# Kernel tuning notes

Hardware: AMD Instinct MI355X
Metric: run time of the kernel (lower is better)

## Reference

```python
import jax, jax.numpy as jnp
import numpy as np
import math

B, T, E, K, V = 64, 512, 512, 512, 512


def setup_inputs() -> dict:
    key = jax.random.key(0)
    ks = jax.random.split(key, 7)
    s = 1.0 / math.sqrt(E)
    return {
        "x": jax.random.normal(ks[0], (B, T, E), dtype=jnp.float32),
        "Wq": jax.random.normal(ks[1], (E, K), dtype=jnp.float32) * s,
        "bq": jnp.zeros((K,), dtype=jnp.float32),
        "Wk": jax.random.normal(ks[2], (E, K), dtype=jnp.float32) * s,
        "bk": jnp.zeros((K,), dtype=jnp.float32),
        "Wv": jax.random.normal(ks[3], (E, V), dtype=jnp.float32) * s,
        "bv": jnp.zeros((V,), dtype=jnp.float32),
    }


def reference(x, Wq, bq, Wk, bk, Wv, bv):
    # Linear projections (N, T, E) -> (N, T, K/V)
    q = x @ Wq + bq
    k = x @ Wk + bk
    v = x @ Wv + bv
    # weight_pos_graph(query, keys) interpreted as Q K^T: (N, T, T)
    scores = jnp.einsum("btd,bsd->bts", q, k)
    # mask[j, i] = 1 if i > j  -> strict upper triangle masked to -inf (causal)
    mask = jnp.triu(jnp.ones((T, T), dtype=bool), k=1)
    scores = jnp.where(mask, -jnp.inf, scores)
    # NOTE: original softmaxes over dim=1 (the query/row axis), not dim=-1
    attn = jax.nn.softmax(scores / math.sqrt(K), axis=1)
    # bmm(attn, values): (N, T, T) @ (N, T, V) -> (N, T, V)
    return jnp.einsum("bts,bsv->btv", attn, v)
```

## Files before the change

kernel.cpp:

```cpp
#include <hip/hip_runtime.h>
#include <hip/hip_bf16.h>
#include <math.h>

#define B_DIM 64
#define T_DIM 512
#define E_DIM 512

typedef __bf16 bf16_t;
typedef bf16_t bf16x8 __attribute__((ext_vector_type(8)));
typedef float  f32x4  __attribute__((ext_vector_type(4)));

typedef unsigned char __attribute__((address_space(1))) uc_g;
typedef unsigned char __attribute__((address_space(3))) uc_l;

__device__ __forceinline__ void gl_lds16(const void* g, void* l) {
  __builtin_amdgcn_global_load_lds((const uc_g*)g, (uc_l*)l, 16, 0, 0);
}

__global__ __launch_bounds__(256)
void prep_kernel(const float* __restrict__ x,
                 const float* __restrict__ Wq, const float* __restrict__ Wk,
                 const float* __restrict__ Wv,
                 const float* __restrict__ bq, const float* __restrict__ bk,
                 const float* __restrict__ bv,
                 bf16_t* __restrict__ xb, bf16_t* __restrict__ WTall,
                 float* __restrict__ bcat, float* __restrict__ Dsum) {
  __shared__ float tile[32][33];
  const int bx = blockIdx.x;
  const int t = threadIdx.x;
  if (bx < 8192) {
    const size_t i = (size_t)bx * 256 + t;
    const float4 a = ((const float4*)x)[i * 2];
    const float4 b = ((const float4*)x)[i * 2 + 1];
    bf16x8 o;
    o[0] = (bf16_t)a.x; o[1] = (bf16_t)a.y; o[2] = (bf16_t)a.z; o[3] = (bf16_t)a.w;
    o[4] = (bf16_t)b.x; o[5] = (bf16_t)b.y; o[6] = (bf16_t)b.z; o[7] = (bf16_t)b.w;
    *(bf16x8*)(xb + i * 8) = o;
  } else if (bx < 8960) {
    const int bid = bx - 8192;
    const int z = bid >> 8;
    const int tl = bid & 255;
    const int c0 = (tl & 15) * 32, r0 = (tl >> 4) * 32;
    const float* W = z == 0 ? Wq : (z == 1 ? Wk : Wv);
    bf16_t* O = WTall + (size_t)z * 512 * E_DIM;
    const int tx = t & 31, ty = t >> 5;
#pragma unroll
    for (int i = 0; i < 4; ++i)
      tile[ty + i * 8][tx] = W[(size_t)(r0 + ty + i * 8) * E_DIM + c0 + tx];
    __syncthreads();
#pragma unroll
    for (int i = 0; i < 4; ++i)
      O[(size_t)(c0 + ty + i * 8) * E_DIM + r0 + tx] = (bf16_t)tile[tx][ty + i * 8];
  } else if (bx == 8960) {
#pragma unroll
    for (int i = t; i < 1536; i += 256)
      bcat[i] = i < 512 ? bq[i] : (i < 1024 ? bk[i - 512] : bv[i - 1024]);
  } else {
    const int i = (bx - 8961) * 256 + t;
    ((float4*)Dsum)[i] = make_float4(0.f, 0.f, 0.f, 0.f);
  }
}

__global__ __launch_bounds__(512) void vtr_kernel(const bf16_t* __restrict__ Vb,
                                                  const float* __restrict__ Dsum,
                                                  bf16_t* __restrict__ VT, int ldv) {
  const int b = blockIdx.z;
  __shared__ bf16_t tile[64][65];
  const int tx = threadIdx.x, ty = threadIdx.y;
  const bf16_t* src = Vb + (size_t)b * T_DIM * ldv;
  const float* Ds = Dsum + (size_t)b * T_DIM;
  bf16_t* dst = VT + (size_t)b * T_DIM * T_DIM;
  const int r0 = blockIdx.y * 64, c0 = blockIdx.x * 64;
#pragma unroll
  for (int i = 0; i < 8; ++i) {
    const int s = r0 + ty + i * 8;
    const float inv = 1.0f / Ds[s];
    tile[ty + i * 8][tx] = (bf16_t)((float)src[(size_t)s * ldv + c0 + tx] * inv);
  }
  __syncthreads();
#pragma unroll
  for (int i = 0; i < 8; ++i)
    dst[(size_t)(c0 + ty + i * 8) * T_DIM + r0 + tx] = tile[tx][ty + i * 8];
}

__global__ __launch_bounds__(512)
void gemm8p_qkv(const bf16_t* __restrict__ A, const bf16_t* __restrict__ Bt,
                bf16_t* __restrict__ C, const float* __restrict__ bias) {
  __shared__ bf16_t lds[65536];
  const int tid = threadIdx.x;

  const int lin = blockIdx.x;
  const int nl = (lin & 7) * 96 + (lin >> 3);
  const int bm = nl / 6, bn = nl - bm * 6;

  const int sg = (tid & 3) ^ ((tid >> 3) & 3);
  const bf16_t* gA = A + ((long)bm * 256 + (tid >> 2)) * 512 + sg * 8;
  const bf16_t* gB = Bt + ((long)bn * 256 + (tid >> 2)) * 512 + sg * 8;

#define STG(T, regoff, gp, kh) {                                          \
    bf16_t* d_ = &lds[(((T) & 1) << 15) + (regoff) + tid * 8];            \
    gl_lds16((gp) + (long)(T) * 64 + (kh) * 32, d_);                      \
    gl_lds16((gp) + (long)(T) * 64 + (kh) * 32 + (long)128 * 512, d_ + 4096); }
#define STG_Ak0(T) STG(T, 0,     gA, 0)
#define STG_Ak1(T) STG(T, 8192,  gA, 1)
#define STG_Bk0(T) STG(T, 16384, gB, 0)
#define STG_Bk1(T) STG(T, 24576, gB, 1)

  const int l15 = tid & 15, lk = (tid >> 4) & 3;
  const int w = tid >> 6, wr = w >> 2, wc = w & 3;
  int aoffs[8], boffs[4];
#pragma unroll
  for (int mm = 0; mm < 8; ++mm) {
    const int row = wr * 128 + mm * 16 + l15;
    aoffs[mm] = row * 32 + (lk ^ ((row >> 1) & 3)) * 8;
  }
#pragma unroll
  for (int n = 0; n < 4; ++n) {
    const int row = wc * 64 + n * 16 + l15;
    boffs[n] = row * 32 + (lk ^ ((row >> 1) & 3)) * 8;
  }

  f32x4 acc[8][4] = {};

  STG_Bk0(0); STG_Ak0(0); STG_Bk1(0); STG_Ak1(0);
  STG_Bk0(1); STG_Ak0(1); STG_Bk1(1);
  asm volatile("s_waitcnt vmcnt(6)" ::: "memory");
  asm volatile("s_barrier" ::: "memory");

#define MFMA16(BASE, AF, BF)                                                    \
  __builtin_amdgcn_s_setprio(1);                                                \
  _Pragma("unroll") for (int m_ = 0; m_ < 4; ++m_)                              \
    _Pragma("unroll") for (int n_ = 0; n_ < 4; ++n_)                            \
      acc[(BASE) + m_][n_] =                                                    \
        __builtin_amdgcn_mfma_f32_16x16x32_bf16(AF[m_], BF[n_], acc[(BASE) + m_][n_], 0, 0, 0); \
  __builtin_amdgcn_s_setprio(0);

  for (int kt = 0; kt < 8; ++kt) {
    const int bb = (kt & 1) << 15;
    bf16x8 a[4], b0[4], b1[4];

#pragma unroll
    for (int n = 0; n < 4; ++n) b0[n] = *(const bf16x8*)&lds[bb + 16384 + boffs[n]];
#pragma unroll
    for (int m = 0; m < 4; ++m) a[m] = *(const bf16x8*)&lds[bb + aoffs[m]];
    if (kt + 1 < 8) STG_Ak1(kt + 1);
    asm volatile("s_barrier" ::: "memory");
    MFMA16(0, a, b0);
    asm volatile("s_barrier" ::: "memory");

#pragma unroll
    for (int m = 0; m < 4; ++m) a[m] = *(const bf16x8*)&lds[bb + aoffs[4 + m]];
    if (kt + 2 < 8) STG_Bk0(kt + 2);
    asm volatile("s_barrier" ::: "memory");
    MFMA16(4, a, b0);
    asm volatile("s_barrier" ::: "memory");

#pragma unroll
    for (int n = 0; n < 4; ++n) b1[n] = *(const bf16x8*)&lds[bb + 24576 + boffs[n]];
#pragma unroll
    for (int m = 0; m < 4; ++m) a[m] = *(const bf16x8*)&lds[bb + 8192 + aoffs[m]];
    if (kt + 2 < 8) STG_Ak0(kt + 2);
    asm volatile("s_barrier" ::: "memory");
    MFMA16(0, a, b1);
    asm volatile("s_barrier" ::: "memory");

#pragma unroll
    for (int m = 0; m < 4; ++m) a[m] = *(const bf16x8*)&lds[bb + 8192 + aoffs[4 + m]];
    if (kt + 2 < 8) {
      STG_Bk1(kt + 2);
      asm volatile("s_waitcnt vmcnt(6)" ::: "memory");
    } else if (kt + 1 < 8) {
      asm volatile("s_waitcnt vmcnt(0)" ::: "memory");
    }
    asm volatile("s_barrier" ::: "memory");
    MFMA16(4, a, b1);
    asm volatile("s_barrier" ::: "memory");
  }
#undef MFMA16
#undef STG_Ak0
#undef STG_Ak1
#undef STG_Bk0
#undef STG_Bk1
#undef STG

#pragma unroll
  for (int mm = 0; mm < 8; ++mm) {
    const long row0 = (long)bm * 256 + wr * 128 + mm * 16 + lk * 4;
#pragma unroll
    for (int n = 0; n < 4; ++n) {
      const int col = bn * 256 + wc * 64 + n * 16 + l15;
      const float bv = bias[col];
#pragma unroll
      for (int r = 0; r < 4; ++r)
        C[(row0 + r) * 1536 + col] = (bf16_t)(acc[mm][n][r] + bv);
    }
  }
}

template <int EPI>
__global__ __launch_bounds__(512)
void gemm_p(const bf16_t* __restrict__ A, const bf16_t* __restrict__ Bt,
            void* __restrict__ Cv, const float* __restrict__ bias,
            float* __restrict__ Dsum,
            int lda, int ldb, int ldc, long sA, long sB, long sC, float scale) {
  __shared__ bf16_t lds[3][12288];
  const int tid = threadIdx.x;

  int bm, bn, bz, NT;
  bm = blockIdx.x; bn = blockIdx.y; bz = blockIdx.z;
  if (EPI == 1 && 2 * bn > bm) return;
  NT = (EPI == 2) ? (bm + 1) * 4 : 16;

  const bf16_t* Ab = A + bz * sA + (long)bm * 128 * lda;
  const bf16_t* Bb = Bt + bz * sB + (long)bn * 256 * ldb;

  const int strow = tid >> 2, stg = tid & 3;
  const int sgg = stg ^ ((strow >> 1) & 3);
  const bf16_t* gA  = Ab + (long)strow * lda + sgg * 8;
  const bf16_t* gB0 = Bb + (long)strow * ldb + sgg * 8;
  const bf16_t* gB1 = gB0 + (long)128 * ldb;

#define STAGE(kt, buf) { gl_lds16(gA  + (long)(kt) * 32, &lds[buf][tid * 8]);        \
                         gl_lds16(gB0 + (long)(kt) * 32, &lds[buf][4096 + tid * 8]); \
                         gl_lds16(gB1 + (long)(kt) * 32, &lds[buf][8192 + tid * 8]); }

  const int l15 = tid & 15, lk = (tid >> 4) & 3;
  const int w = tid >> 6, wr = w >> 2, wc = w & 3;
  int aoff[4], boff[4];
#pragma unroll
  for (int m = 0; m < 4; ++m) {
    const int row = wr * 64 + m * 16 + l15;
    aoff[m] = row * 32 + (lk ^ ((row >> 1) & 3)) * 8;
  }
#pragma unroll
  for (int n = 0; n < 4; ++n) {
    const int row = wc * 64 + n * 16 + l15;
    boff[n] = 4096 + row * 32 + (lk ^ ((row >> 1) & 3)) * 8;
  }

  f32x4 acc[4][4] = {};

  STAGE(0, 0); STAGE(1, 1);
  asm volatile("s_waitcnt vmcnt(3)" ::: "memory");
  asm volatile("s_barrier" ::: "memory");

  int cb = 0;
  for (int kt = 0; kt < NT; ++kt) {
    bf16x8 af[4], bfr[4];
#pragma unroll
    for (int m = 0; m < 4; ++m) af[m] = *(const bf16x8*)&lds[cb][aoff[m]];
#pragma unroll
    for (int n = 0; n < 4; ++n) bfr[n] = *(const bf16x8*)&lds[cb][boff[n]];
    const int sb = (cb == 0) ? 2 : cb - 1;
    if (kt + 2 < NT) {
      STAGE(kt + 2, sb);
      asm volatile("s_waitcnt vmcnt(3)" ::: "memory");
    } else if (kt + 2 == NT) {
      asm volatile("s_waitcnt vmcnt(0)" ::: "memory");
    }
    asm volatile("s_barrier" ::: "memory");
    __builtin_amdgcn_s_setprio(1);
#pragma unroll
    for (int m = 0; m < 4; ++m)
#pragma unroll
      for (int n = 0; n < 4; ++n)
        acc[m][n] = __builtin_amdgcn_mfma_f32_16x16x32_bf16(af[m], bfr[n], acc[m][n], 0, 0, 0);
    __builtin_amdgcn_s_setprio(0);
    asm volatile("s_barrier" ::: "memory");
    cb = (cb == 2) ? 0 : cb + 1;
  }
#undef STAGE

  if constexpr (EPI == 1) {
    bf16_t* C = (bf16_t*)Cv + bz * sC;
    float ts[4] = {0.f, 0.f, 0.f, 0.f};
#pragma unroll
    for (int m = 0; m < 4; ++m) {
      const long row0 = (long)bm * 128 + wr * 64 + m * 16 + lk * 4;
#pragma unroll
      for (int n = 0; n < 4; ++n) {
        const int col = bn * 256 + wc * 64 + n * 16 + l15;
#pragma unroll
        for (int r = 0; r < 4; ++r) {
          const long row = row0 + r;
          float e = 0.f;
          if (col <= row) e = __expf(acc[m][n][r] * scale);
          const bf16_t eb = (bf16_t)e;
          C[row * (long)ldc + col] = eb;
          ts[n] += (float)eb;
        }
      }
    }
#pragma unroll
    for (int n = 0; n < 4; ++n) {
      ts[n] += __shfl_xor(ts[n], 16);
      ts[n] += __shfl_xor(ts[n], 32);
    }
    float* colsum = (float*)&lds[0][0];
    if (tid < 256) colsum[tid] = 0.f;
    __syncthreads();
    if (lk == 0) {
#pragma unroll
      for (int n = 0; n < 4; ++n)
        atomicAdd(&colsum[wc * 64 + n * 16 + l15], ts[n]);
    }
    __syncthreads();
    if (tid < 256)
      atomicAdd(&Dsum[(long)bz * T_DIM + bn * 256 + tid], colsum[tid]);
  } else {
    float* C = (float*)Cv + bz * sC;
#pragma unroll
    for (int m = 0; m < 4; ++m) {
      const long row0 = (long)bm * 128 + wr * 64 + m * 16 + lk * 4;
#pragma unroll
      for (int n = 0; n < 4; ++n) {
        const int col = bn * 256 + wc * 64 + n * 16 + l15;
#pragma unroll
        for (int r = 0; r < 4; ++r)
          C[(row0 + r) * (long)ldc + col] = acc[m][n][r];
      }
    }
  }
}

extern "C" void kernel_launch(void* const* d_in, const int* in_sizes, int n_in,
                              void* d_out, int out_size, void* d_ws, size_t ws_size,
                              hipStream_t stream) {
  const float* x  = (const float*)d_in[0];
  const float* Wq = (const float*)d_in[1];
  const float* bq = (const float*)d_in[2];
  const float* Wk = (const float*)d_in[3];
  const float* bk = (const float*)d_in[4];
  const float* Wv = (const float*)d_in[5];
  const float* bv = (const float*)d_in[6];
  float* out = (float*)d_out;

  char* ws = (char*)d_ws;
  const size_t SZ = (size_t)B_DIM * T_DIM * E_DIM * 2;
  bf16_t* xb    = (bf16_t*)(ws);
  bf16_t* P     = (bf16_t*)(ws);
  bf16_t* qkv   = (bf16_t*)(ws + SZ);
  bf16_t* vT    = (bf16_t*)(ws + SZ + 3 * SZ);
  bf16_t* WTall = (bf16_t*)(ws + 5 * SZ);
  float*  bcat  = (float*)(ws + 5 * SZ + 1572864);
  float*  Dsum  = (float*)(ws + 5 * SZ + 1572864 + 8192);

  const long sQKV = (long)T_DIM * 1536;
  const long bstr = (long)T_DIM * T_DIM;
  const float scale = 1.0f / sqrtf((float)E_DIM);

  prep_kernel<<<dim3(8993), dim3(256), 0, stream>>>(
      x, Wq, Wk, Wv, bq, bk, bv, xb, WTall, bcat, Dsum);
  gemm8p_qkv<<<dim3(768), dim3(512), 0, stream>>>(xb, WTall, qkv, bcat);
  gemm_p<1><<<dim3(4, 2, B_DIM), dim3(512), 0, stream>>>(
      qkv, qkv + 512, P, nullptr, Dsum, 1536, 1536, T_DIM, sQKV, sQKV, bstr, scale);
  vtr_kernel<<<dim3(8, 8, B_DIM), dim3(64, 8), 0, stream>>>(qkv + 1024, Dsum, vT, 1536);
  gemm_p<2><<<dim3(4, 2, B_DIM), dim3(512), 0, stream>>>(
      P, vT, out, nullptr, nullptr, 512, 512, T_DIM, bstr, bstr, bstr, 1.f);
}
```

Baseline: 273.5 us.

## Fuse column softmax normalization into scores kernel and write V transposed from projection

The scores kernel now computes all 512 query rows for a 128-key column block per workgroup. This lets it reduce column sums in LDS and normalize P directly, with no global Dsum atomics and no separate normalization pass. The projection GEMM switches to 128x256 tiles with a 3-buffer pipeline and writes the V slice transposed directly into vT, which removes the vtr_kernel launch and its extra read/write pass. The cost is that upper-triangle waves sit idle in the scores kernel, and there are only 256 scores workgroups, which lowers occupancy.

```diff
diff --git a/kernel.cpp b/kernel.cpp
--- a/kernel.cpp
+++ b/kernel.cpp
@@ -8,6 +8,7 @@
 
 typedef __bf16 bf16_t;
 typedef bf16_t bf16x8 __attribute__((ext_vector_type(8)));
+typedef bf16_t bf16x4 __attribute__((ext_vector_type(4)));
 typedef float  f32x4  __attribute__((ext_vector_type(4)));
 
 typedef unsigned char __attribute__((address_space(1))) uc_g;
@@ -24,7 +25,7 @@
                  const float* __restrict__ bq, const float* __restrict__ bk,
                  const float* __restrict__ bv,
                  bf16_t* __restrict__ xb, bf16_t* __restrict__ WTall,
-                 float* __restrict__ bcat, float* __restrict__ Dsum) {
+                 float* __restrict__ bcat) {
   __shared__ float tile[32][33];
   const int bx = blockIdx.x;
   const int t = threadIdx.x;
@@ -51,63 +52,141 @@
 #pragma unroll
     for (int i = 0; i < 4; ++i)
       O[(size_t)(c0 + ty + i * 8) * E_DIM + r0 + tx] = (bf16_t)tile[tx][ty + i * 8];
-  } else if (bx == 8960) {
+  } else {
 #pragma unroll
     for (int i = t; i < 1536; i += 256)
       bcat[i] = i < 512 ? bq[i] : (i < 1024 ? bk[i - 512] : bv[i - 1024]);
-  } else {
-    const int i = (bx - 8961) * 256 + t;
-    ((float4*)Dsum)[i] = make_float4(0.f, 0.f, 0.f, 0.f);
-  }
-}
-
-__global__ __launch_bounds__(512) void vtr_kernel(const bf16_t* __restrict__ Vb,
-                                                  const float* __restrict__ Dsum,
-                                                  bf16_t* __restrict__ VT, int ldv) {
-  const int b = blockIdx.z;
-  __shared__ bf16_t tile[64][65];
-  const int tx = threadIdx.x, ty = threadIdx.y;
-  const bf16_t* src = Vb + (size_t)b * T_DIM * ldv;
-  const float* Ds = Dsum + (size_t)b * T_DIM;
-  bf16_t* dst = VT + (size_t)b * T_DIM * T_DIM;
-  const int r0 = blockIdx.y * 64, c0 = blockIdx.x * 64;
-#pragma unroll
-  for (int i = 0; i < 8; ++i) {
-    const int s = r0 + ty + i * 8;
-    const float inv = 1.0f / Ds[s];
-    tile[ty + i * 8][tx] = (bf16_t)((float)src[(size_t)s * ldv + c0 + tx] * inv);
-  }
-  __syncthreads();
-#pragma unroll
-  for (int i = 0; i < 8; ++i)
-    dst[(size_t)(c0 + ty + i * 8) * T_DIM + r0 + tx] = tile[tx][ty + i * 8];
+  }
 }
 
 __global__ __launch_bounds__(512)
-void gemm8p_qkv(const bf16_t* __restrict__ A, const bf16_t* __restrict__ Bt,
-                bf16_t* __restrict__ C, const float* __restrict__ bias) {
-  __shared__ bf16_t lds[65536];
+void proj_kernel(const bf16_t* __restrict__ A, const bf16_t* __restrict__ Bt,
+                 bf16_t* __restrict__ qkv, bf16_t* __restrict__ vT,
+                 const float* __restrict__ bias) {
+  __shared__ bf16_t lds[3][12288];
   const int tid = threadIdx.x;
 
   const int lin = blockIdx.x;
-  const int nl = (lin & 7) * 96 + (lin >> 3);
+  const int nl = (lin & 7) * 192 + (lin >> 3);
   const int bm = nl / 6, bn = nl - bm * 6;
 
-  const int sg = (tid & 3) ^ ((tid >> 3) & 3);
-  const bf16_t* gA = A + ((long)bm * 256 + (tid >> 2)) * 512 + sg * 8;
-  const bf16_t* gB = Bt + ((long)bn * 256 + (tid >> 2)) * 512 + sg * 8;
-
-#define STG(T, regoff, gp, kh) {                                          \
-    bf16_t* d_ = &lds[(((T) & 1) << 15) + (regoff) + tid * 8];            \
-    gl_lds16((gp) + (long)(T) * 64 + (kh) * 32, d_);                      \
-    gl_lds16((gp) + (long)(T) * 64 + (kh) * 32 + (long)128 * 512, d_ + 4096); }
-#define STG_Ak0(T) STG(T, 0,     gA, 0)
-#define STG_Ak1(T) STG(T, 8192,  gA, 1)
-#define STG_Bk0(T) STG(T, 16384, gB, 0)
-#define STG_Bk1(T) STG(T, 24576, gB, 1)
+  const bf16_t* Ab = A + (long)bm * 128 * 512;
+  const bf16_t* Bb = Bt + (long)bn * 256 * 512;
+
+  const int strow = tid >> 2, stg = tid & 3;
+  const int sgg = stg ^ ((strow >> 1) & 3);
+  const bf16_t* gA  = Ab + (long)strow * 512 + sgg * 8;
+  const bf16_t* gB0 = Bb + (long)strow * 512 + sgg * 8;
+  const bf16_t* gB1 = gB0 + (long)128 * 512;
+
+#define STAGE(kt, buf) { gl_lds16(gA  + (long)(kt) * 32, &lds[buf][tid * 8]);        \
+                         gl_lds16(gB0 + (long)(kt) * 32, &lds[buf][4096 + tid * 8]); \
+                         gl_lds16(gB1 + (long)(kt) * 32, &lds[buf][8192 + tid * 8]); }
 
   const int l15 = tid & 15, lk = (tid >> 4) & 3;
   const int w = tid >> 6, wr = w >> 2, wc = w & 3;
+  int aoff[4], boff[4];
+#pragma unroll
+  for (int m = 0; m < 4; ++m) {
+    const int row = wr * 64 + m * 16 + l15;
+    aoff[m] = row * 32 + (lk ^ ((row >> 1) & 3)) * 8;
+  }
+#pragma unroll
+  for (int n = 0; n < 4; ++n) {
+    const int row = wc * 64 + n * 16 + l15;
+    boff[n] = 4096 + row * 32 + (lk ^ ((row >> 1) & 3)) * 8;
+  }
+
+  f32x4 acc[4][4] = {};
+
+  STAGE(0, 0); STAGE(1, 1);
+  asm volatile("s_waitcnt vmcnt(3)" ::: "memory");
+  asm volatile("s_barrier" ::: "memory");
+
+  int cb = 0;
+  for (int kt = 0; kt < 16; ++kt) {
+    bf16x8 af[4], bfr[4];
+#pragma unroll
+    for (int m = 0; m < 4; ++m) af[m] = *(const bf16x8*)&lds[cb][aoff[m]];
+#pragma unroll
+    for (int n = 0; n < 4; ++n) bfr[n] = *(const bf16x8*)&lds[cb][boff[n]];
+    const int sb = (cb == 0) ? 2 : cb - 1;
+    if (kt + 2 < 16) {
+      STAGE(kt + 2, sb);
+      asm volatile("s_waitcnt vmcnt(3)" ::: "memory");
+    } else if (kt + 2 == 16) {
+      asm volatile("s_waitcnt vmcnt(0)" ::: "memory");
+    }
+    asm volatile("s_barrier" ::: "memory");
+    __builtin_amdgcn_s_setprio(1);
+#pragma unroll
+    for (int m = 0; m < 4; ++m)
+#pragma unroll
+      for (int n = 0; n < 4; ++n)
+        acc[m][n] = __builtin_amdgcn_mfma_f32_16x16x32_bf16(af[m], bfr[n], acc[m][n], 0, 0, 0);
+    __builtin_amdgcn_s_setprio(0);
+    asm volatile("s_barrier" ::: "memory");
+    cb = (cb == 2) ? 0 : cb + 1;
+  }
+#undef STAGE
+
+  if (bn < 4) {
+#pragma unroll
+    for (int m = 0; m < 4; ++m) {
+      const long row0 = (long)bm * 128 + wr * 64 + m * 16 + lk * 4;
+#pragma unroll
+      for (int n = 0; n < 4; ++n) {
+        const int col = bn * 256 + wc * 64 + n * 16 + l15;
+        const float bv = bias[col];
+#pragma unroll
+        for (int r = 0; r < 4; ++r)
+          qkv[(row0 + r) * 1536L + col] = (bf16_t)(acc[m][n][r] + bv);
+      }
+    }
+  } else {
+#pragma unroll
+    for (int m = 0; m < 4; ++m) {
+      const long row0 = (long)bm * 128 + wr * 64 + m * 16 + lk * 4;
+      const long b = row0 >> 9;
+      const int s0 = (int)(row0 & 511);
+#pragma unroll
+      for (int n = 0; n < 4; ++n) {
+        const int col = bn * 256 + wc * 64 + n * 16 + l15;
+        const float bv = bias[col];
+        const int vc = col - 1024;
+        bf16x4 o;
+#pragma unroll
+        for (int r = 0; r < 4; ++r) o[r] = (bf16_t)(acc[m][n][r] + bv);
+        *(bf16x4*)(vT + b * 262144 + (long)vc * 512 + s0) = o;
+      }
+    }
+  }
+}
+
+__global__ __launch_bounds__(512)
+void scores_kernel(const bf16_t* __restrict__ qkv, bf16_t* __restrict__ P,
+                   float scale) {
+  __shared__ bf16_t lds[3][20480];
+  const int tid = threadIdx.x;
+  const int bn = blockIdx.x;
+  const int bz = blockIdx.y;
+  const bf16_t* q = qkv + (long)bz * T_DIM * 1536;
+  const bf16_t* k = q + 512;
+
+  const int strow = tid >> 2, stg = tid & 3;
+  const int sg = stg ^ ((strow >> 1) & 3);
+  const bf16_t* gA = q + (long)strow * 1536 + sg * 8;
+  const bf16_t* gB = k + ((long)bn * 128 + strow) * 1536 + sg * 8;
+
+#define STAGE(kt, buf) {                                                            \
+    _Pragma("unroll") for (int i_ = 0; i_ < 4; ++i_)                                \
+      gl_lds16(gA + (long)(kt) * 32 + (long)i_ * 128 * 1536,                        \
+               &lds[buf][i_ * 4096 + tid * 8]);                                     \
+    gl_lds16(gB + (long)(kt) * 32, &lds[buf][16384 + tid * 8]); }
+
+  const int l15 = tid & 15, lk = (tid >> 4) & 3;
+  const int w = tid >> 6, wr = w >> 1, wc = w & 1;
+  const int active = (wr >= bn);
   int aoffs[8], boffs[4];
 #pragma unroll
   for (int mm = 0; mm < 8; ++mm) {
@@ -117,108 +196,116 @@
 #pragma unroll
   for (int n = 0; n < 4; ++n) {
     const int row = wc * 64 + n * 16 + l15;
-    boffs[n] = row * 32 + (lk ^ ((row >> 1) & 3)) * 8;
+    boffs[n] = 16384 + row * 32 + (lk ^ ((row >> 1) & 3)) * 8;
   }
 
   f32x4 acc[8][4] = {};
 
-  STG_Bk0(0); STG_Ak0(0); STG_Bk1(0); STG_Ak1(0);
-  STG_Bk0(1); STG_Ak0(1); STG_Bk1(1);
-  asm volatile("s_waitcnt vmcnt(6)" ::: "memory");
+  STAGE(0, 0); STAGE(1, 1);
+  asm volatile("s_waitcnt vmcnt(5)" ::: "memory");
   asm volatile("s_barrier" ::: "memory");
 
-#define MFMA16(BASE, AF, BF)                                                    \
-  __builtin_amdgcn_s_setprio(1);                                                \
-  _Pragma("unroll") for (int m_ = 0; m_ < 4; ++m_)                              \
-    _Pragma("unroll") for (int n_ = 0; n_ < 4; ++n_)                            \
-      acc[(BASE) + m_][n_] =                                                    \
-        __builtin_amdgcn_mfma_f32_16x16x32_bf16(AF[m_], BF[n_], acc[(BASE) + m_][n_], 0, 0, 0); \
-  __builtin_amdgcn_s_setprio(0);
-
-  for (int kt = 0; kt < 8; ++kt) {
-    const int bb = (kt & 1) << 15;
-    bf16x8 a[4], b0[4], b1[4];
-
-#pragma unroll
-    for (int n = 0; n < 4; ++n) b0[n] = *(const bf16x8*)&lds[bb + 16384 + boffs[n]];
-#pragma unroll
-    for (int m = 0; m < 4; ++m) a[m] = *(const bf16x8*)&lds[bb + aoffs[m]];
-    if (kt + 1 < 8) STG_Ak1(kt + 1);
-    asm volatile("s_barrier" ::: "memory");
-    MFMA16(0, a, b0);
-    asm volatile("s_barrier" ::: "memory");
-
-#pragma unroll
-    for (int m = 0; m < 4; ++m) a[m] = *(const bf16x8*)&lds[bb + aoffs[4 + m]];
-    if (kt + 2 < 8) STG_Bk0(kt + 2);
-    asm volatile("s_barrier" ::: "memory");
-    MFMA16(4, a, b0);
-    asm volatile("s_barrier" ::: "memory");
-
-#pragma unroll
-    for (int n = 0; n < 4; ++n) b1[n] = *(const bf16x8*)&lds[bb + 24576 + boffs[n]];
-#pragma unroll
-    for (int m = 0; m < 4; ++m) a[m] = *(const bf16x8*)&lds[bb + 8192 + aoffs[m]];
-    if (kt + 2 < 8) STG_Ak0(kt + 2);
-    asm volatile("s_barrier" ::: "memory");
-    MFMA16(0, a, b1);
-    asm volatile("s_barrier" ::: "memory");
-
-#pragma unroll
-    for (int m = 0; m < 4; ++m) a[m] = *(const bf16x8*)&lds[bb + 8192 + aoffs[4 + m]];
-    if (kt + 2 < 8) {
-      STG_Bk1(kt + 2);
-      asm volatile("s_waitcnt vmcnt(6)" ::: "memory");
-    } else if (kt + 1 < 8) {
+  int cb = 0;
+  for (int kt = 0; kt < 16; ++kt) {
+    bf16x8 af[8], bfr[4];
+    if (active) {
+#pragma unroll
+      for (int mm = 0; mm < 8; ++mm) af[mm] = *(const bf16x8*)&lds[cb][aoffs[mm]];
+#pragma unroll
+      for (int n = 0; n < 4; ++n) bfr[n] = *(const bf16x8*)&lds[cb][boffs[n]];
+    }
+    const int sb = (cb == 0) ? 2 : cb - 1;
+    if (kt + 2 < 16) {
+      STAGE(kt + 2, sb);
+      asm volatile("s_waitcnt vmcnt(5)" ::: "memory");
+    } else if (kt + 2 == 16) {
       asm volatile("s_waitcnt vmcnt(0)" ::: "memory");
     }
     asm volatile("s_barrier" ::: "memory");
-    MFMA16(4, a, b1);
-    asm volatile("s_barrier" ::: "memory");
-  }
-#undef MFMA16
-#undef STG_Ak0
-#undef STG_Ak1
-#undef STG_Bk0
-#undef STG_Bk1
-#undef STG
-
-#pragma unroll
-  for (int mm = 0; mm < 8; ++mm) {
-    const long row0 = (long)bm * 256 + wr * 128 + mm * 16 + lk * 4;
+    if (active) {
+      __builtin_amdgcn_s_setprio(1);
+#pragma unroll
+      for (int mm = 0; mm < 8; ++mm)
+#pragma unroll
+        for (int n = 0; n < 4; ++n)
+          acc[mm][n] = __builtin_amdgcn_mfma_f32_16x16x32_bf16(af[mm], bfr[n], acc[mm][n], 0, 0, 0);
+      __builtin_amdgcn_s_setprio(0);
+    }
+    asm volatile("s_barrier" ::: "memory");
+    cb = (cb == 2) ? 0 : cb + 1;
+  }
+#undef STAGE
+
+  float* colsum = (float*)&lds[0][0];
+  if (tid < 128) colsum[tid] = 0.f;
+  __syncthreads();
+
+  float ts[4] = {0.f, 0.f, 0.f, 0.f};
+  if (active) {
+#pragma unroll
+    for (int mm = 0; mm < 8; ++mm) {
+      const int trow = wr * 128 + mm * 16 + lk * 4;
+#pragma unroll
+      for (int n = 0; n < 4; ++n) {
+        const int scol = bn * 128 + wc * 64 + n * 16 + l15;
+#pragma unroll
+        for (int r = 0; r < 4; ++r) {
+          float e = 0.f;
+          if (scol <= trow + r) e = __expf(acc[mm][n][r] * scale);
+          acc[mm][n][r] = e;
+          ts[n] += e;
+        }
+      }
+    }
 #pragma unroll
     for (int n = 0; n < 4; ++n) {
-      const int col = bn * 256 + wc * 64 + n * 16 + l15;
-      const float bv = bias[col];
-#pragma unroll
-      for (int r = 0; r < 4; ++r)
-        C[(row0 + r) * 1536 + col] = (bf16_t)(acc[mm][n][r] + bv);
-    }
-  }
-}
-
-template <int EPI>
+      ts[n] += __shfl_xor(ts[n], 16);
+      ts[n] += __shfl_xor(ts[n], 32);
+    }
+    if (lk == 0) {
+#pragma unroll
+      for (int n = 0; n < 4; ++n)
+        atomicAdd(&colsum[wc * 64 + n * 16 + l15], ts[n]);
+    }
+  }
+  __syncthreads();
+
+  if (active) {
+    bf16_t* Pb = P + (long)bz * 262144;
+    float inv[4];
+#pragma unroll
+    for (int n = 0; n < 4; ++n)
+      inv[n] = 1.0f / colsum[wc * 64 + n * 16 + l15];
+#pragma unroll
+    for (int mm = 0; mm < 8; ++mm) {
+      const int trow = wr * 128 + mm * 16 + lk * 4;
+#pragma unroll
+      for (int n = 0; n < 4; ++n) {
+        const int scol = bn * 128 + wc * 64 + n * 16 + l15;
+#pragma unroll
+        for (int r = 0; r < 4; ++r)
+          Pb[(long)(trow + r) * 512 + scol] = (bf16_t)(acc[mm][n][r] * inv[n]);
+      }
+    }
+  }
+}
+
 __global__ __launch_bounds__(512)
-void gemm_p(const bf16_t* __restrict__ A, const bf16_t* __restrict__ Bt,
-            void* __restrict__ Cv, const float* __restrict__ bias,
-            float* __restrict__ Dsum,
-            int lda, int ldb, int ldc, long sA, long sB, long sC, float scale) {
+void pv_kernel(const bf16_t* __restrict__ Pn, const bf16_t* __restrict__ vT,
+               float* __restrict__ out) {
   __shared__ bf16_t lds[3][12288];
   const int tid = threadIdx.x;
-
-  int bm, bn, bz, NT;
-  bm = blockIdx.x; bn = blockIdx.y; bz = blockIdx.z;
-  if (EPI == 1 && 2 * bn > bm) return;
-  NT = (EPI == 2) ? (bm + 1) * 4 : 16;
-
-  const bf16_t* Ab = A + bz * sA + (long)bm * 128 * lda;
-  const bf16_t* Bb = Bt + bz * sB + (long)bn * 256 * ldb;
+  const int bm = blockIdx.x, bn = blockIdx.y, bz = blockIdx.z;
+  const int NT = (bm + 1) * 4;
+
+  const bf16_t* Ab = Pn + (long)bz * 262144 + (long)bm * 128 * 512;
+  const bf16_t* Bb = vT + (long)bz * 262144 + (long)bn * 256 * 512;
 
   const int strow = tid >> 2, stg = tid & 3;
   const int sgg = stg ^ ((strow >> 1) & 3);
-  const bf16_t* gA  = Ab + (long)strow * lda + sgg * 8;
-  const bf16_t* gB0 = Bb + (long)strow * ldb + sgg * 8;
-  const bf16_t* gB1 = gB0 + (long)128 * ldb;
+  const bf16_t* gA  = Ab + (long)strow * 512 + sgg * 8;
+  const bf16_t* gB0 = Bb + (long)strow * 512 + sgg * 8;
+  const bf16_t* gB1 = gB0 + (long)128 * 512;
 
 #define STAGE(kt, buf) { gl_lds16(gA  + (long)(kt) * 32, &lds[buf][tid * 8]);        \
                          gl_lds16(gB0 + (long)(kt) * 32, &lds[buf][4096 + tid * 8]); \
@@ -240,7 +327,8 @@
 
   f32x4 acc[4][4] = {};
 
-  STAGE(0, 0); STAGE(1, 1);
+  STAGE(0, 0);
+  if (NT > 1) STAGE(1, 1);
   asm volatile("s_waitcnt vmcnt(3)" ::: "memory");
   asm volatile("s_barrier" ::: "memory");
 
@@ -271,54 +359,16 @@
   }
 #undef STAGE
 
-  if constexpr (EPI == 1) {
-    bf16_t* C = (bf16_t*)Cv + bz * sC;
-    float ts[4] = {0.f, 0.f, 0.f, 0.f};
-#pragma unroll
-    for (int m = 0; m < 4; ++m) {
-      const long row0 = (long)bm * 128 + wr * 64 + m * 16 + lk * 4;
-#pragma unroll
-      for (int n = 0; n < 4; ++n) {
-        const int col = bn * 256 + wc * 64 + n * 16 + l15;
-#pragma unroll
-        for (int r = 0; r < 4; ++r) {
-          const long row = row0 + r;
-          float e = 0.f;
-          if (col <= row) e = __expf(acc[m][n][r] * scale);
-          const bf16_t eb = (bf16_t)e;
-          C[row * (long)ldc + col] = eb;
-          ts[n] += (float)eb;
-        }
-      }
-    }
+  float* C = out + (long)bz * 262144;
+#pragma unroll
+  for (int m = 0; m < 4; ++m) {
+    const long row0 = (long)bm * 128 + wr * 64 + m * 16 + lk * 4;
 #pragma unroll
     for (int n = 0; n < 4; ++n) {
-      ts[n] += __shfl_xor(ts[n], 16);
-      ts[n] += __shfl_xor(ts[n], 32);
-    }
-    float* colsum = (float*)&lds[0][0];
-    if (tid < 256) colsum[tid] = 0.f;
-    __syncthreads();
-    if (lk == 0) {
-#pragma unroll
-      for (int n = 0; n < 4; ++n)
-        atomicAdd(&colsum[wc * 64 + n * 16 + l15], ts[n]);
-    }
-    __syncthreads();
-    if (tid < 256)
-      atomicAdd(&Dsum[(long)bz * T_DIM + bn * 256 + tid], colsum[tid]);
-  } else {
-    float* C = (float*)Cv + bz * sC;
-#pragma unroll
-    for (int m = 0; m < 4; ++m) {
-      const long row0 = (long)bm * 128 + wr * 64 + m * 16 + lk * 4;
-#pragma unroll
-      for (int n = 0; n < 4; ++n) {
-        const int col = bn * 256 + wc * 64 + n * 16 + l15;
-#pragma unroll
-        for (int r = 0; r < 4; ++r)
-          C[(row0 + r) * (long)ldc + col] = acc[m][n][r];
-      }
+      const int col = bn * 256 + wc * 64 + n * 16 + l15;
+#pragma unroll
+      for (int r = 0; r < 4; ++r)
+        C[(row0 + r) * 512 + col] = acc[m][n][r];
     }
   }
 }
@@ -340,21 +390,15 @@
   bf16_t* xb    = (bf16_t*)(ws);
   bf16_t* P     = (bf16_t*)(ws);
   bf16_t* qkv   = (bf16_t*)(ws + SZ);
-  bf16_t* vT    = (bf16_t*)(ws + SZ + 3 * SZ);
+  bf16_t* vT    = (bf16_t*)(ws + 4 * SZ);
   bf16_t* WTall = (bf16_t*)(ws + 5 * SZ);
   float*  bcat  = (float*)(ws + 5 * SZ + 1572864);
-  float*  Dsum  = (float*)(ws + 5 * SZ + 1572864 + 8192);
-
-  const long sQKV = (long)T_DIM * 1536;
-  const long bstr = (long)T_DIM * T_DIM;
+
   const float scale = 1.0f / sqrtf((float)E_DIM);
 
-  prep_kernel<<<dim3(8993), dim3(256), 0, stream>>>(
-      x, Wq, Wk, Wv, bq, bk, bv, xb, WTall, bcat, Dsum);
-  gemm8p_qkv<<<dim3(768), dim3(512), 0, stream>>>(xb, WTall, qkv, bcat);
-  gemm_p<1><<<dim3(4, 2, B_DIM), dim3(512), 0, stream>>>(
-      qkv, qkv + 512, P, nullptr, Dsum, 1536, 1536, T_DIM, sQKV, sQKV, bstr, scale);
-  vtr_kernel<<<dim3(8, 8, B_DIM), dim3(64, 8), 0, stream>>>(qkv + 1024, Dsum, vT, 1536);
-  gemm_p<2><<<dim3(4, 2, B_DIM), dim3(512), 0, stream>>>(
-      P, vT, out, nullptr, nullptr, 512, 512, T_DIM, bstr, bstr, bstr, 1.f);
-}
+  prep_kernel<<<dim3(8961), dim3(256), 0, stream>>>(
+      x, Wq, Wk, Wv, bq, bk, bv, xb, WTall, bcat);
+  proj_kernel<<<dim3(1536), dim3(512), 0, stream>>>(xb, WTall, qkv, vT, bcat);
+  scores_kernel<<<dim3(4, B_DIM), dim3(512), 0, stream>>>(qkv, P, scale);
+  pv_kernel<<<dim3(4, 2, B_DIM), dim3(512), 0, stream>>>(P, vT, out);
+}
```

Result: faster. 261.2 us (-4.5%).
